# Optimization experiments

Hardware: AMD Instinct MI355X
Metric: run time of the kernel (lower is better)

The kernel has to match this reference:

```python
import jax, jax.numpy as jnp
import numpy as np

B, S, D = 4, 1024, 1024
DB = 128           # d_bottleneck (router embedding dim)
R = 128            # neuron bottleneck rank
N_QK, N_V, N_KNOW = 2048, 2048, 4096
MB_QK, MB_V, MB_KNOW = 16, 16, 32
H = 16
EPS = 1e-8


def _unit(k, shape):
    v = jax.random.normal(k, shape, jnp.float32)
    return v / (jnp.linalg.norm(v, axis=-1, keepdims=True) + EPS)


def setup_inputs() -> dict:
    key = jax.random.key(0)
    ks = jax.random.split(key, 16)
    s = 0.02
    nrm = lambda k, sh, sc=0.02: jax.random.normal(k, sh, jnp.float32) * sc
    return {
        "x": jax.random.normal(ks[0], (B, S, D), jnp.float32),
        "qk_emb": _unit(ks[1], (N_QK, DB)),
        "v_emb": _unit(ks[2], (N_V, DB)),
        "know_emb": _unit(ks[3], (N_KNOW, DB)),
        "qk_f": nrm(ks[4], (MB_QK, D, R)),
        "qk_r": nrm(ks[5], (MB_QK, R, D)),
        "v_f": nrm(ks[6], (MB_V, D, R)),
        "v_r": nrm(ks[7], (MB_V, R, D)),
        "know_f": nrm(ks[8], (MB_KNOW, D, R)),
        "know_r": nrm(ks[9], (MB_KNOW, R, D)),
        "proj_attn_k": nrm(ks[10], (D, 3 * DB)),
        "proj_attn_b": jnp.zeros((3 * DB,), jnp.float32),
        "tau_attn_k": nrm(ks[11], (D, 3)),
        "tau_attn_b": jnp.zeros((3,), jnp.float32),
        "proj_know_k": nrm(ks[12], (D, DB)),
        "proj_know_b": jnp.zeros((DB,), jnp.float32),
        "tau_know_k": nrm(ks[13], (D, 1)),
        "tau_know_b": jnp.zeros((1,), jnp.float32),
        "expand_O": nrm(ks[14], (D, D)),
        "ln1_scale": jnp.ones((D,), jnp.float32),
        "ln1_bias": jnp.zeros((D,), jnp.float32),
        "ln2_scale": jnp.ones((D,), jnp.float32),
        "ln2_bias": jnp.zeros((D,), jnp.float32),
    }


def layer_norm(x, scale, bias, eps=1e-6):
    mean = jnp.mean(x, axis=-1, keepdims=True)
    var = jnp.mean(jnp.square(x - mean), axis=-1, keepdims=True)
    return (x - mean) / jnp.sqrt(var + eps) * scale + bias


def threshold_gate(scores, tau):
    gate = jnp.maximum(scores - tau, 0.0)
    return gate / (gate.sum(axis=-1, keepdims=True) + EPS)


def group_gate(gate, n_basis):
    b, s, n = gate.shape  # n divisible by n_basis here
    g = gate.reshape(b, s, n_basis, n // n_basis).sum(axis=-1)
    return g / (g.sum(axis=-1, keepdims=True) + EPS)


@jax.checkpoint
def feature_fn(x, neurons, weights):
    all_h = jnp.einsum('bsd,ndr->bsnr', x, neurons)
    return jnp.einsum('bsnr,bsn->bsr', all_h, weights)


@jax.checkpoint
def restore_fn(h, neurons, weights):
    pre = jnp.einsum('bsr,bsn->bsnr', h, weights)
    return jnp.einsum('bsnr,nrd->bsd', pre, neurons)


def reference(x, qk_emb, v_emb, know_emb, qk_f, qk_r, v_f, v_r, know_f, know_r,
              proj_attn_k, proj_attn_b, tau_attn_k, tau_attn_b,
              proj_know_k, proj_know_b, tau_know_k, tau_know_b,
              expand_O, ln1_scale, ln1_bias, ln2_scale, ln2_bias):
    # ---- attention circuit (pre-LN) ----
    n1 = layer_norm(x, ln1_scale, ln1_bias)
    qk_n = qk_emb / (jnp.linalg.norm(qk_emb, axis=-1, keepdims=True) + EPS)
    v_n = v_emb / (jnp.linalg.norm(v_emb, axis=-1, keepdims=True) + EPS)
    h_all = n1 @ proj_attn_k + proj_attn_b            # [B,S,3*DB]
    h_q, h_k, h_v = jnp.split(h_all, 3, axis=-1)
    tau = n1 @ tau_attn_k + tau_attn_b                # [B,S,3]
    g_q = threshold_gate(h_q @ qk_n.T, tau[:, :, 0:1])
    g_k = threshold_gate(h_k @ qk_n.T, tau[:, :, 1:2])
    g_v = threshold_gate(h_v @ v_n.T, tau[:, :, 2:3])
    gq_b = group_gate(g_q, MB_QK)
    gk_b = group_gate(g_k, MB_QK)
    gv_b = group_gate(g_v, MB_V)
    Q = restore_fn(feature_fn(n1, qk_f, gq_b), qk_r, gq_b)
    K = restore_fn(feature_fn(n1, qk_f, gk_b), qk_r, gk_b)
    V = restore_fn(feature_fn(n1, v_f, gv_b), v_r, gv_b)
    d_head = D // H
    Q = Q.reshape(B, S, H, d_head).transpose(0, 2, 1, 3)
    K = K.reshape(B, S, H, d_head).transpose(0, 2, 1, 3)
    V = V.reshape(B, S, H, d_head).transpose(0, 2, 1, 3)
    scores = jnp.einsum('bhsd,bhtd->bhst', Q, K) / jnp.sqrt(jnp.float32(d_head))
    causal = jnp.tril(jnp.ones((S, S), dtype=jnp.bool_))
    scores = jnp.where(causal, scores, jnp.finfo(scores.dtype).min)
    attn_w = jax.nn.softmax(scores, axis=-1)
    attn_out = jnp.einsum('bhst,bhtd->bhsd', attn_w, V)
    attn_out = attn_out.transpose(0, 2, 1, 3).reshape(B, S, D) @ expand_O
    t_qk, t_v = 1.0 / N_QK, 1.0 / N_V
    a_aux = (((g_q.mean(axis=(0, 1)) - t_qk) ** 2).sum() * N_QK +
             ((g_k.mean(axis=(0, 1)) - t_qk) ** 2).sum() * N_QK +
             ((g_v.mean(axis=(0, 1)) - t_v) ** 2).sum() * N_V)
    x = x + attn_out
    # ---- knowledge circuit (pre-LN) ----
    n2 = layer_norm(x, ln2_scale, ln2_bias)
    know_n = know_emb / (jnp.linalg.norm(know_emb, axis=-1, keepdims=True) + EPS)
    h = n2 @ proj_know_k + proj_know_b
    tau_k = n2 @ tau_know_k + tau_know_b
    gate = threshold_gate(h @ know_n.T, tau_k)
    g_b = group_gate(gate, MB_KNOW)
    know_out = restore_fn(feature_fn(n2, know_f, g_b), know_r, g_b)
    k_aux = ((gate.mean(axis=(0, 1)) - 1.0 / N_KNOW) ** 2).sum() * N_KNOW
    x = x + know_out
    return x, a_aux + k_aux
```

## Files before the change

kernel.cpp:

```cpp
#include <hip/hip_runtime.h>
#include <math.h>

static constexpr int T = 4096;
static constexpr int D = 1024;

typedef __bf16 bf16_t;
typedef bf16_t bf16x8 __attribute__((ext_vector_type(8)));
typedef bf16_t bf16x4 __attribute__((ext_vector_type(4)));
typedef float f32x4 __attribute__((ext_vector_type(4)));

#define GLDS16(g, l)                                                        \
  __builtin_amdgcn_global_load_lds(                                         \
      (const __attribute__((address_space(1))) void*)(g),                   \
      (__attribute__((address_space(3))) void*)(l), 16, 0, 0)


__global__ void zero1_kernel(float* p) { *p = 0.f; }

__global__ __launch_bounds__(256) void ln_kernel(
    const float* __restrict__ x, const float* __restrict__ scale,
    const float* __restrict__ bias, float* __restrict__ out_f,
    bf16_t* __restrict__ out_b)
{
  int t = blockIdx.x;
  const float* xr = x + (size_t)t * D;
  float v[4];
  float s1 = 0.f, s2 = 0.f;
#pragma unroll
  for (int i = 0; i < 4; i++) {
    v[i] = xr[threadIdx.x + i * 256];
    s1 += v[i];
    s2 += v[i] * v[i];
  }
#pragma unroll
  for (int o = 1; o < 64; o <<= 1) {
    s1 += __shfl_xor(s1, o);
    s2 += __shfl_xor(s2, o);
  }
  __shared__ float r1[4], r2[4];
  int wid = threadIdx.x >> 6;
  if ((threadIdx.x & 63) == 0) { r1[wid] = s1; r2[wid] = s2; }
  __syncthreads();
  s1 = r1[0] + r1[1] + r1[2] + r1[3];
  s2 = r2[0] + r2[1] + r2[2] + r2[3];
  float mean = s1 * (1.f / D);
  float var = s2 * (1.f / D) - mean * mean;
  float rstd = rsqrtf(var + 1e-6f);
  float* orow = out_f + (size_t)t * D;
  bf16_t* brow = out_b + (size_t)t * D;
#pragma unroll
  for (int i = 0; i < 4; i++) {
    int d = threadIdx.x + i * 256;
    float o = (v[i] - mean) * rstd * scale[d] + bias[d];
    orow[d] = o;
    brow[d] = (bf16_t)o;
  }
}

__global__ __launch_bounds__(64) void norm_rows_kernel(
    const float* __restrict__ e, bf16_t* __restrict__ o)
{
  int r = blockIdx.x;
  const float* row = e + (size_t)r * 128;
  float a = row[threadIdx.x], b = row[threadIdx.x + 64];
  float ss = a * a + b * b;
#pragma unroll
  for (int m = 1; m < 64; m <<= 1) ss += __shfl_xor(ss, m);
  float inv = 1.f / (sqrtf(ss) + 1e-8f);
  bf16_t* orow = o + (size_t)r * 128;
  orow[threadIdx.x] = (bf16_t)(a * inv);
  orow[threadIdx.x + 64] = (bf16_t)(b * inv);
}

__global__ __launch_bounds__(64) void tau_kernel(
    const float* __restrict__ n, const float* __restrict__ W,
    const float* __restrict__ b, float* __restrict__ out, int J)
{
  int t = blockIdx.x;
  const float* nr = n + (size_t)t * D;
  for (int j = 0; j < J; j++) {
    float p = 0.f;
#pragma unroll 4
    for (int i = 0; i < 16; i++) {
      int d = threadIdx.x + i * 64;
      p += nr[d] * W[d * J + j];
    }
#pragma unroll
    for (int m = 1; m < 64; m <<= 1) p += __shfl_xor(p, m);
    if (threadIdx.x == 0) out[t * J + j] = p + b[j];
  }
}

template <int PER>
__device__ __forceinline__ void gate_body(
    float* __restrict__ row, float tv, float* __restrict__ gb, int G)
{
  float r[PER];
  int base = threadIdx.x * PER;
  float psum = 0.f;
#pragma unroll
  for (int i = 0; i < PER; i++) {
    float s = row[base + i] - tv;
    s = fmaxf(s, 0.f);
    r[i] = s;
    psum += s;
  }
  __shared__ float red[4];
  __shared__ float grp[32];
  if (threadIdx.x < 32) grp[threadIdx.x] = 0.f;
  float w = psum;
#pragma unroll
  for (int m = 1; m < 64; m <<= 1) w += __shfl_xor(w, m);
  int wid = threadIdx.x >> 6;
  if ((threadIdx.x & 63) == 0) red[wid] = w;
  __syncthreads();
  float Stot = red[0] + red[1] + red[2] + red[3];
  atomicAdd(&grp[base >> 7], psum);
  __syncthreads();
  float inv = 1.f / (Stot + 1e-8f);
#pragma unroll
  for (int i = 0; i < PER; i++) row[base + i] = r[i] * inv;
  if (threadIdx.x < G) {
    float Gj = grp[threadIdx.x] * inv;
    float gsum = Stot * inv;
    gb[threadIdx.x] = Gj / (gsum + 1e-8f);
  }
}

template <int PER>
__global__ __launch_bounds__(256) void gate_kernel(
    float* __restrict__ g, const float* __restrict__ tau, int tauStride,
    int tauOff, float* __restrict__ gb, int N, int G)
{
  int t = blockIdx.x;
  gate_body<PER>(g + (size_t)t * N, tau[t * tauStride + tauOff],
                 gb + (size_t)t * G, G);
}

template <int PER>
__global__ __launch_bounds__(256) void gate3_kernel(
    float* __restrict__ s0, float* __restrict__ s1, float* __restrict__ s2,
    const float* __restrict__ tau, float* __restrict__ g0,
    float* __restrict__ g1, float* __restrict__ g2, int N, int G)
{
  int t = blockIdx.x, y = blockIdx.y;
  float* g = y == 0 ? s0 : y == 1 ? s1 : s2;
  float* gb = y == 0 ? g0 : y == 1 ? g1 : g2;
  gate_body<PER>(g + (size_t)t * N, tau[t * 3 + y], gb + (size_t)t * G, G);
}

__global__ __launch_bounds__(256) void colsum_part_kernel(
    const float* __restrict__ g, int N, float* __restrict__ colsum)
{
  int c = blockIdx.x * 256 + threadIdx.x;
  int r0 = blockIdx.y * 128;
  const float* p = g + (size_t)r0 * N + c;
  float s = 0.f;
#pragma unroll 8
  for (int t = 0; t < 128; t++) s += p[(size_t)t * N];
  atomicAdd(&colsum[c], s);
}

__global__ __launch_bounds__(256) void colsum_part3_kernel(
    const float* __restrict__ s0, const float* __restrict__ s1,
    const float* __restrict__ s2, int N, float* __restrict__ colsum)
{
  int z = blockIdx.z;
  const float* g = z == 0 ? s0 : z == 1 ? s1 : s2;
  int c = blockIdx.x * 256 + threadIdx.x;
  int r0 = blockIdx.y * 128;
  const float* p = g + (size_t)r0 * N + c;
  float s = 0.f;
#pragma unroll 8
  for (int t = 0; t < 128; t++) s += p[(size_t)t * N];
  atomicAdd(&colsum[z * N + c], s);
}

__global__ __launch_bounds__(256) void colsum_fin_kernel(
    const float* __restrict__ colsum, int N, float tinv,
    float* __restrict__ aux)
{
  int c = blockIdx.x * 256 + threadIdx.x;
  float mdev = colsum[c] * (1.f / T) - tinv;
  float p = mdev * mdev * (float)N;
#pragma unroll
  for (int m = 1; m < 64; m <<= 1) p += __shfl_xor(p, m);
  __shared__ float red[4];
  if ((threadIdx.x & 63) == 0) red[threadIdx.x >> 6] = p;
  __syncthreads();
  if (threadIdx.x == 0) atomicAdd(aux, red[0] + red[1] + red[2] + red[3]);
}

__global__ __launch_bounds__(128) void wsum2_kernel(
    const bf16_t* __restrict__ all_h, const float* __restrict__ gb1,
    const float* __restrict__ gb2, float* __restrict__ h1,
    float* __restrict__ h2, int NB)
{
  int t = blockIdx.x;
  int r = threadIdx.x;
  const bf16_t* row = all_h + (size_t)t * NB * 128;
  float a1 = 0.f, a2 = 0.f;
  for (int n = 0; n < NB; n++) {
    float v = (float)row[n * 128 + r];
    a1 += gb1[(size_t)t * NB + n] * v;
    if (gb2) a2 += gb2[(size_t)t * NB + n] * v;
  }
  h1[(size_t)t * 128 + r] = a1;
  if (h2) h2[(size_t)t * 128 + r] = a2;
}

__global__ __launch_bounds__(128) void wsum2b_kernel(
    const bf16_t* __restrict__ aq, const bf16_t* __restrict__ av,
    const float* __restrict__ gq, const float* __restrict__ gk,
    const float* __restrict__ gv, float* __restrict__ hQ,
    float* __restrict__ hK, float* __restrict__ hV, int NB)
{
  int t = blockIdx.x, y = blockIdx.y;
  int r = threadIdx.x;
  const bf16_t* row = (y == 0 ? aq : av) + (size_t)t * NB * 128;
  const float* g1 = (y == 0 ? gq : gv) + (size_t)t * NB;
  const float* g2 = y == 0 ? gk + (size_t)t * NB : nullptr;
  float a1 = 0.f, a2 = 0.f;
  for (int n = 0; n < NB; n++) {
    float v = (float)row[n * 128 + r];
    a1 += g1[n] * v;
    if (g2) a2 += g2[n] * v;
  }
  if (y == 0) {
    hQ[(size_t)t * 128 + r] = a1;
    hK[(size_t)t * 128 + r] = a2;
  } else {
    hV[(size_t)t * 128 + r] = a1;
  }
}

__global__ __launch_bounds__(256) void transpose_to_bf16_kernel(
    const float* __restrict__ src, bf16_t* __restrict__ dst,
    int R, int C, size_t sbs, size_t dbs)
{
  __shared__ float tile[32][33];
  int b = blockIdx.z;
  int c0 = blockIdx.x * 32, r0 = blockIdx.y * 32;
  int tx = threadIdx.x & 31, ty = threadIdx.x >> 5;
  const float* s = src + (size_t)b * sbs;
  bf16_t* d = dst + (size_t)b * dbs;
#pragma unroll
  for (int i = 0; i < 4; i++)
    tile[ty + i * 8][tx] = s[(size_t)(r0 + ty + i * 8) * C + c0 + tx];
  __syncthreads();
#pragma unroll
  for (int i = 0; i < 4; i++)
    d[(size_t)(c0 + ty + i * 8) * R + r0 + tx] = (bf16_t)tile[tx][ty + i * 8];
}

__device__ __forceinline__ void avirt_body(
    const float* hr, const float* gr, bf16_t* ar, int K)
{
  int noct = K >> 3;
  for (int o = threadIdx.x; o < noct; o += 256) {
    int k = o * 8;
    float g = gr[k >> 7];
    bf16x8 v;
#pragma unroll
    for (int i = 0; i < 8; i++) v[i] = (bf16_t)(hr[(k & 127) + i] * g);
    *(bf16x8*)(ar + k) = v;
  }
}

__global__ __launch_bounds__(256) void avirt_kernel(
    const float* __restrict__ h, const float* __restrict__ gb, int NB,
    bf16_t* __restrict__ A, int K)
{
  int t = blockIdx.x;
  avirt_body(h + (size_t)t * 128, gb + (size_t)t * NB, A + (size_t)t * K, K);
}

__global__ __launch_bounds__(256) void avirt3_kernel(
    const float* __restrict__ h0, const float* __restrict__ h1,
    const float* __restrict__ h2, const float* __restrict__ g0,
    const float* __restrict__ g1, const float* __restrict__ g2, int NB,
    bf16_t* __restrict__ A0, bf16_t* __restrict__ A1,
    bf16_t* __restrict__ A2, int K)
{
  int t = blockIdx.x, y = blockIdx.y;
  const float* h = y == 0 ? h0 : y == 1 ? h1 : h2;
  const float* g = y == 0 ? g0 : y == 1 ? g1 : g2;
  bf16_t* A = y == 0 ? A0 : y == 1 ? A1 : A2;
  avirt_body(h + (size_t)t * 128, g + (size_t)t * NB, A + (size_t)t * K, K);
}

__global__ __launch_bounds__(256) void combine2_kernel(
    const float* __restrict__ p0, const float* __restrict__ p1,
    float* __restrict__ out)
{
  int i = blockIdx.x * 256 + threadIdx.x;
  float4 a = ((const float4*)p0)[i];
  float4 b = ((const float4*)p1)[i];
  float4 o = ((float4*)out)[i];
  o.x += a.x + b.x;
  o.y += a.y + b.y;
  o.z += a.z + b.z;
  o.w += a.w + b.w;
  ((float4*)out)[i] = o;
}

template <bool HAS_BIAS, bool HAS_RESID>
__device__ __forceinline__ void gemm_store(
    int mode, void* Cv, int ldc, const float* bias, const float* resid,
    int ldr, int rowb, int col, const f32x4& a)
{
  if (mode == 2) {
    bf16x4 v4;
#pragma unroll
    for (int r = 0; r < 4; r++) v4[r] = (bf16_t)a[r];
    bf16_t* dst = (bf16_t*)Cv +
        ((size_t)(rowb >> 10) * 1024 + col) * 1024 + (rowb & 1023);
    *(bf16x4*)dst = v4;
  } else {
#pragma unroll
    for (int r = 0; r < 4; r++) {
      int row = rowb + r;
      float v = a[r];
      if (HAS_BIAS) v += bias[col];
      if (HAS_RESID) v += resid[(size_t)row * ldr + col];
      if (mode == 1)
        ((bf16_t*)Cv)[(size_t)row * ldc + col] = (bf16_t)v;
      else
        ((float*)Cv)[(size_t)row * ldc + col] = v;
    }
  }
}

template <bool HAS_BIAS, bool HAS_RESID, int OUT_MODE>
__global__ __launch_bounds__(256) void mfma_gemm_kernel(
    const bf16_t* __restrict__ A, int lda,
    const bf16_t* __restrict__ Bt, int ldb,
    void* __restrict__ Cv, int ldc,
    const float* __restrict__ bias,
    const float* __restrict__ resid, int ldr,
    int M, int N, int K)
{
  __shared__ bf16_t As[2][64 * 32];
  __shared__ bf16_t Bs[2][128 * 32];
  int tid = threadIdx.x;
  int wave = tid >> 6, lane = tid & 63;

  unsigned lid = blockIdx.y * gridDim.x + blockIdx.x;
  unsigned nwg = gridDim.x * gridDim.y;
  unsigned swzb = lid;
  if ((nwg & 7u) == 0u) swzb = (lid & 7u) * (nwg >> 3) + (lid >> 3);
  int row0 = (int)(swzb / gridDim.x) * 64;
  int col0 = (int)(swzb % gridDim.x) * 128;

  int wr = (wave >> 1) * 32, wc = (wave & 1) * 64;
  f32x4 acc[2][4] = {};

  int srow = (wave << 4) + (lane >> 2);
  int g8 = (((lane & 3) ^ ((srow >> 1) & 3)) << 3);
  const bf16_t* gA = A + (size_t)(row0 + srow) * lda + g8;
  const bf16_t* gB = Bt + (size_t)(col0 + srow) * ldb + g8;
  size_t b64 = (size_t)64 * ldb;

  int fr = lane & 15, fq = lane >> 4;

#define GSTAGE(buf, k0s)                                  \
  {                                                       \
    GLDS16(gA + (k0s), &As[buf][wave * 512]);             \
    GLDS16(gB + (k0s), &Bs[buf][wave * 512]);             \
    GLDS16(gB + b64 + (k0s), &Bs[buf][2048 + wave * 512]);\
  }

  GSTAGE(0, 0);
  int cur = 0;
  for (int k0 = 0; k0 < K; k0 += 32) {
    __syncthreads();
    if (k0 + 32 < K) GSTAGE(cur ^ 1, k0 + 32);
    bf16x8 af[2], bfr[4];
#pragma unroll
    for (int m = 0; m < 2; m++) {
      int R = wr + m * 16 + fr;
      af[m] = *(const bf16x8*)&As[cur][R * 32 + ((fq ^ ((R >> 1) & 3)) << 3)];
    }
#pragma unroll
    for (int n = 0; n < 4; n++) {
      int R = wc + n * 16 + fr;
      bfr[n] = *(const bf16x8*)&Bs[cur][R * 32 + ((fq ^ ((R >> 1) & 3)) << 3)];
    }
#pragma unroll
    for (int m = 0; m < 2; m++)
#pragma unroll
      for (int n = 0; n < 4; n++)
        acc[m][n] = __builtin_amdgcn_mfma_f32_16x16x32_bf16(af[m], bfr[n],
                                                            acc[m][n], 0, 0, 0);
    cur ^= 1;
  }
#undef GSTAGE

#pragma unroll
  for (int m = 0; m < 2; m++)
#pragma unroll
    for (int n = 0; n < 4; n++)
      gemm_store<HAS_BIAS, HAS_RESID>(
          OUT_MODE, Cv, ldc, bias, resid, ldr,
          row0 + wr + m * 16 + fq * 4, col0 + wc + n * 16 + fr, acc[m][n]);
}

struct ZArg { const bf16_t* A; const bf16_t* Bt; void* C; int mode; };

__device__ __forceinline__ void gemm128_body(
    const bf16_t* __restrict__ A, int lda, const bf16_t* __restrict__ Bt,
    int ldb, void* __restrict__ Cv, int ldc, int mode, int row0, int col0,
    int K)
{
  __shared__ bf16_t As[2][128 * 32];
  __shared__ bf16_t Bs[2][128 * 32];
  int tid = threadIdx.x;
  int wave = tid >> 6, lane = tid & 63;
  int wr = (wave >> 1) * 64, wc = (wave & 1) * 64;
  f32x4 acc[4][4] = {};

  int srow = (wave << 4) + (lane >> 2);
  int g8 = (((lane & 3) ^ ((srow >> 1) & 3)) << 3);
  const bf16_t* gA = A + (size_t)(row0 + srow) * lda + g8;
  const bf16_t* gB = Bt + (size_t)(col0 + srow) * ldb + g8;
  size_t a64 = (size_t)64 * lda, b64 = (size_t)64 * ldb;

  int fr = lane & 15, fq = lane >> 4;

#define GSTAGE8(buf, k0s)                                  \
  {                                                        \
    GLDS16(gA + (k0s), &As[buf][wave * 512]);              \
    GLDS16(gA + a64 + (k0s), &As[buf][2048 + wave * 512]); \
    GLDS16(gB + (k0s), &Bs[buf][wave * 512]);              \
    GLDS16(gB + b64 + (k0s), &Bs[buf][2048 + wave * 512]); \
  }

  GSTAGE8(0, 0);
  int cur = 0;
  for (int k0 = 0; k0 < K; k0 += 32) {
    __syncthreads();
    if (k0 + 32 < K) GSTAGE8(cur ^ 1, k0 + 32);
    bf16x8 af[4], bfr[4];
#pragma unroll
    for (int m = 0; m < 4; m++) {
      int R = wr + m * 16 + fr;
      af[m] = *(const bf16x8*)&As[cur][R * 32 + ((fq ^ ((R >> 1) & 3)) << 3)];
    }
#pragma unroll
    for (int n = 0; n < 4; n++) {
      int R = wc + n * 16 + fr;
      bfr[n] = *(const bf16x8*)&Bs[cur][R * 32 + ((fq ^ ((R >> 1) & 3)) << 3)];
    }
#pragma unroll
    for (int m = 0; m < 4; m++)
#pragma unroll
      for (int n = 0; n < 4; n++)
        acc[m][n] = __builtin_amdgcn_mfma_f32_16x16x32_bf16(af[m], bfr[n],
                                                            acc[m][n], 0, 0, 0);
    cur ^= 1;
  }
#undef GSTAGE8

#pragma unroll
  for (int m = 0; m < 4; m++)
#pragma unroll
    for (int n = 0; n < 4; n++)
      gemm_store<false, false>(
          mode, Cv, ldc, nullptr, nullptr, 0,
          row0 + wr + m * 16 + fq * 4, col0 + wc + n * 16 + fr, acc[m][n]);
}

template <int OUT_MODE>
__global__ __launch_bounds__(256) void mfma_gemm128_kernel(
    const bf16_t* __restrict__ A, int lda,
    const bf16_t* __restrict__ Bt, int ldb,
    void* __restrict__ Cv, int ldc, int K)
{
  unsigned lid = blockIdx.y * gridDim.x + blockIdx.x;
  unsigned nwg = gridDim.x * gridDim.y;
  unsigned swzb = lid;
  if ((nwg & 7u) == 0u) swzb = (lid & 7u) * (nwg >> 3) + (lid >> 3);
  int row0 = (int)(swzb / gridDim.x) * 128;
  int col0 = (int)(swzb % gridDim.x) * 128;
  gemm128_body(A, lda, Bt, ldb, Cv, ldc, OUT_MODE, row0, col0, K);
}

__global__ __launch_bounds__(256) void mfma_gemm128b_kernel(
    ZArg za, ZArg zb, ZArg zc, int lda, int ldb, int ldc, int K)
{
  unsigned gx = gridDim.x;
  unsigned gxy = gridDim.x * gridDim.y;
  unsigned lid = (blockIdx.z * gridDim.y + blockIdx.y) * gx + blockIdx.x;
  unsigned nwg = gxy * gridDim.z;
  unsigned swzb = lid;
  if ((nwg & 7u) == 0u) swzb = (lid & 7u) * (nwg >> 3) + (lid >> 3);
  unsigned zi = swzb / gxy;
  unsigned rem = swzb % gxy;
  int row0 = (int)(rem / gx) * 128;
  int col0 = (int)(rem % gx) * 128;
  ZArg Z = (zi == 0) ? za : (zi == 1) ? zb : zc;
  gemm128_body(Z.A, lda, Z.Bt, ldb, Z.C, ldc, Z.mode, row0, col0, K);
}

__global__ __launch_bounds__(512) void flash_mfma_kernel(
    const bf16_t* __restrict__ Q, const bf16_t* __restrict__ K,
    const bf16_t* __restrict__ Vt, bf16_t* __restrict__ O)
{
  __shared__ bf16_t Ks[2][64 * 64];
  __shared__ bf16_t Vs[2][64 * 64];
  __shared__ bf16_t Pl[8][32 * 64];

  int tid = threadIdx.x;
  int wave = tid >> 6, lane = tid & 63;
  int fr = lane & 15, fq = lane >> 4;
  unsigned lid = blockIdx.x + blockIdx.y * 4 + blockIdx.z * 64;
  unsigned swz8 = (lid & 7u) * 32 + (lid >> 3);
  int s_slot = swz8 & 3;
  unsigned hb = swz8 >> 2;
  int h = hb & 15, b = hb >> 4;
  int half = wave >> 2, w4 = wave & 3;
  int qb = half ? (7 - s_slot) : s_slot;
  int q0w = qb * 128 + w4 * 32;
  int KT = 16 - 2 * s_slot;
  size_t qkbase = ((size_t)b * 1024) * 1024 + (size_t)h * 64;
  size_t vtbase = ((size_t)b * 1024 + (size_t)h * 64) * 1024;

  int srow8 = lane >> 3;
  int scb = (((lane & 7) << 4) ^ (srow8 << 4)) >> 1;

#define FSTAGE(buf, kt)                                                     \
  {                                                                         \
    int k0s = (kt) * 64;                                                    \
    int row = wave * 8 + srow8;                                             \
    GLDS16(&K[qkbase + (size_t)(k0s + row) * 1024 + scb],                   \
           &Ks[buf][wave * 512]);                                           \
    GLDS16(&Vt[vtbase + (size_t)row * 1024 + k0s + scb],                    \
           &Vs[buf][wave * 512]);                                           \
  }

  bf16x8 qf[2][2];
#pragma unroll
  for (int g = 0; g < 2; g++)
#pragma unroll
    for (int kh = 0; kh < 2; kh++)
      qf[g][kh] = *(const bf16x8*)&Q[qkbase +
                                     (size_t)(q0w + g * 16 + fr) * 1024 +
                                     kh * 32 + fq * 8];

  f32x4 o_acc[2][4] = {};
  float mrow[2][4], lrow[2][4];
#pragma unroll
  for (int g = 0; g < 2; g++)
#pragma unroll
    for (int r = 0; r < 4; r++) { mrow[g][r] = -INFINITY; lrow[g][r] = 0.f; }

  char* P = (char*)&Pl[wave][0];

  FSTAGE(0, 0);

  for (int kt = 0; kt < KT; kt++) {
    __syncthreads();
    if (kt + 1 < KT) FSTAGE((kt + 1) & 1, kt + 1);
    int k0 = kt * 64;
    if (k0 <= q0w + 31) {
      const char* Kb = (const char*)&Ks[kt & 1][0];
      const char* Vb = (const char*)&Vs[kt & 1][0];
      int swz = (fr & 7) << 4;
      f32x4 s[2][4] = {};
#pragma unroll
      for (int n = 0; n < 4; n++) {
        int rowo = (n * 16 + fr) * 128;
        bf16x8 kf0 = *(const bf16x8*)(Kb + rowo + ((fq * 16) ^ swz));
        bf16x8 kf1 = *(const bf16x8*)(Kb + rowo + ((64 + fq * 16) ^ swz));
#pragma unroll
        for (int g = 0; g < 2; g++) {
          s[g][n] = __builtin_amdgcn_mfma_f32_16x16x32_bf16(qf[g][0], kf0,
                                                            s[g][n], 0, 0, 0);
          s[g][n] = __builtin_amdgcn_mfma_f32_16x16x32_bf16(qf[g][1], kf1,
                                                            s[g][n], 0, 0, 0);
        }
      }
      const float scale = 0.125f;
#pragma unroll
      for (int g = 0; g < 2; g++) {
        bool dm = (k0 + 63 > q0w + g * 16);
#pragma unroll
        for (int n = 0; n < 4; n++)
#pragma unroll
          for (int r = 0; r < 4; r++) {
            float v = s[g][n][r] * scale;
            if (dm && (k0 + n * 16 + fr > q0w + g * 16 + fq * 4 + r))
              v = -INFINITY;
            s[g][n][r] = v;
          }
      }
      float corr[2][4];
#pragma unroll
      for (int g = 0; g < 2; g++)
#pragma unroll
        for (int r = 0; r < 4; r++) {
          float mx = fmaxf(fmaxf(s[g][0][r], s[g][1][r]),
                           fmaxf(s[g][2][r], s[g][3][r]));
#pragma unroll
          for (int msk = 1; msk < 16; msk <<= 1)
            mx = fmaxf(mx, __shfl_xor(mx, msk));
          float mnew = fmaxf(mrow[g][r], mx);
          corr[g][r] = __expf(mrow[g][r] - mnew);
          mrow[g][r] = mnew;
          float ps = 0.f;
#pragma unroll
          for (int n = 0; n < 4; n++) {
            float p = __expf(s[g][n][r] - mnew);
            s[g][n][r] = p;
            ps += p;
          }
#pragma unroll
          for (int msk = 1; msk < 16; msk <<= 1) ps += __shfl_xor(ps, msk);
          lrow[g][r] = lrow[g][r] * corr[g][r] + ps;
        }
#pragma unroll
      for (int g = 0; g < 2; g++)
#pragma unroll
        for (int n = 0; n < 4; n++)
#pragma unroll
          for (int r = 0; r < 4; r++) {
            int q = g * 16 + fq * 4 + r;
            int cb = ((n * 16 + fr) * 2) ^ ((q & 7) << 4);
            *(bf16_t*)(P + q * 128 + cb) = (bf16_t)s[g][n][r];
          }
      int rr = fr & 3;
      int srcl = (fr >> 2) << 4;
#pragma unroll
      for (int g = 0; g < 2; g++) {
        float c0 = __shfl(corr[g][0], srcl);
        float c1 = __shfl(corr[g][1], srcl);
        float c2 = __shfl(corr[g][2], srcl);
        float c3 = __shfl(corr[g][3], srcl);
        float cq = rr == 0 ? c0 : rr == 1 ? c1 : rr == 2 ? c2 : c3;
#pragma unroll
        for (int n = 0; n < 4; n++)
#pragma unroll
          for (int r = 0; r < 4; r++) o_acc[g][n][r] *= cq;
      }
#pragma unroll
      for (int c = 0; c < 2; c++) {
        bf16x8 pf[2];
#pragma unroll
        for (int g = 0; g < 2; g++)
          pf[g] = *(const bf16x8*)(P + (g * 16 + fr) * 128 +
                                   ((c * 64 + fq * 16) ^ swz));
#pragma unroll
        for (int n = 0; n < 4; n++) {
          bf16x8 vf = *(const bf16x8*)(Vb + (n * 16 + fr) * 128 +
                                       ((c * 64 + fq * 16) ^ swz));
#pragma unroll
          for (int g = 0; g < 2; g++)
            o_acc[g][n] = __builtin_amdgcn_mfma_f32_16x16x32_bf16(
                vf, pf[g], o_acc[g][n], 0, 0, 0);
        }
      }
    }
  }
  int rr = fr & 3;
  int srcl = (fr >> 2) << 4;
#pragma unroll
  for (int g = 0; g < 2; g++) {
    float l0 = __shfl(lrow[g][0], srcl);
    float l1 = __shfl(lrow[g][1], srcl);
    float l2 = __shfl(lrow[g][2], srcl);
    float l3 = __shfl(lrow[g][3], srcl);
    float lq = rr == 0 ? l0 : rr == 1 ? l1 : rr == 2 ? l2 : l3;
    float linv = 1.f / lq;
    size_t orow = qkbase + (size_t)(q0w + g * 16 + fr) * 1024;
#pragma unroll
    for (int n = 0; n < 4; n++) {
      bf16x4 ov;
#pragma unroll
      for (int r = 0; r < 4; r++) ov[r] = (bf16_t)(o_acc[g][n][r] * linv);
      *(bf16x4*)&O[orow + n * 16 + fq * 4] = ov;
    }
  }
#undef FSTAGE
}


extern "C" void kernel_launch(void* const* d_in, const int* in_sizes, int n_in,
                              void* d_out, int out_size, void* d_ws,
                              size_t ws_size, hipStream_t stream) {
  (void)in_sizes; (void)n_in; (void)out_size; (void)ws_size;
  const float* x          = (const float*)d_in[0];
  const float* qk_emb     = (const float*)d_in[1];
  const float* v_emb      = (const float*)d_in[2];
  const float* know_emb   = (const float*)d_in[3];
  const float* qk_f       = (const float*)d_in[4];
  const float* qk_r       = (const float*)d_in[5];
  const float* v_f        = (const float*)d_in[6];
  const float* v_r        = (const float*)d_in[7];
  const float* know_f     = (const float*)d_in[8];
  const float* know_r     = (const float*)d_in[9];
  const float* proj_attn_k = (const float*)d_in[10];
  const float* proj_attn_b = (const float*)d_in[11];
  const float* tau_attn_k  = (const float*)d_in[12];
  const float* tau_attn_b  = (const float*)d_in[13];
  const float* proj_know_k = (const float*)d_in[14];
  const float* proj_know_b = (const float*)d_in[15];
  const float* tau_know_k  = (const float*)d_in[16];
  const float* tau_know_b  = (const float*)d_in[17];
  const float* expand_O    = (const float*)d_in[18];
  const float* ln1_scale   = (const float*)d_in[19];
  const float* ln1_bias    = (const float*)d_in[20];
  const float* ln2_scale   = (const float*)d_in[21];
  const float* ln2_bias    = (const float*)d_in[22];

  float* out = (float*)d_out;
  float* aux = out + (size_t)T * D;

  float* ws = (float*)d_ws;
  float* n_f   = ws;
  float* tau3  = n_f + 4194304;
  float* gq_b  = tau3 + 16384;
  float* gk_b  = gq_b + 65536;
  float* gv_b  = gk_b + 65536;
  float* gkn_b = gv_b + 65536;
  float* csum  = gkn_b + 131072;
  float* hQ    = csum + 8192;
  float* hK    = hQ + 524288;
  float* hV    = hK + 524288;
  float* qkvarena = hV + 524288;
  float* buf_big = qkvarena + 12582912;

  bf16_t* Qbb = (bf16_t*)qkvarena;
  bf16_t* Kbb = Qbb + (size_t)T * 1024;
  bf16_t* Vtb = Kbb + (size_t)T * 1024;

  bf16_t* nb   = (bf16_t*)(buf_big + 16777216);
  bf16_t* hab  = nb + 4194304;
  bf16_t* embB = hab + 1572864;
  bf16_t* B2t  = embB + 524288;
  bf16_t* wt   = B2t + 4194304;
  bf16_t* pa_t  = wt;
  bf16_t* qkr_t = pa_t + 393216;
  bf16_t* vr_t  = qkr_t + 2097152;
  bf16_t* knr_t = vr_t + 2097152;
  bf16_t* eo_t  = knr_t + 4194304;
  bf16_t* pk_t  = eo_t + 1048576;
  bf16_t* B2t2  = pk_t + 131072;

  float* s_q = buf_big;
  float* s_k = buf_big + 8388608;
  float* s_v = (float*)qkvarena;
  bf16_t* allh_q = (bf16_t*)buf_big;
  bf16_t* allh_v = allh_q + (size_t)T * 2048;
  bf16_t* avbQ = (bf16_t*)buf_big;
  bf16_t* avbK = avbQ + (size_t)T * 2048;
  bf16_t* avbV = avbK + (size_t)T * 2048;
  bf16_t* avbN = (bf16_t*)buf_big;
  bf16_t* allh_n = (bf16_t*)buf_big;
  float* kp0 = buf_big + 8388608;
  float* kp1 = kp0 + 4194304;
  bf16_t* attnb_b = (bf16_t*)(buf_big + 12582912);

  bf16_t* embQ = embB;
  bf16_t* embV = embB + 262144;

  dim3 blk(256);

  zero1_kernel<<<1, 1, 0, stream>>>(aux);

  transpose_to_bf16_kernel<<<dim3(12, 32, 1), blk, 0, stream>>>(
      proj_attn_k, pa_t, 1024, 384, 0, 0);
  transpose_to_bf16_kernel<<<dim3(32, 64, 1), blk, 0, stream>>>(
      qk_r, qkr_t, 2048, 1024, 0, 0);
  transpose_to_bf16_kernel<<<dim3(32, 64, 1), blk, 0, stream>>>(
      v_r, vr_t, 2048, 1024, 0, 0);
  transpose_to_bf16_kernel<<<dim3(32, 128, 1), blk, 0, stream>>>(
      know_r, knr_t, 4096, 1024, 0, 0);
  transpose_to_bf16_kernel<<<dim3(32, 32, 1), blk, 0, stream>>>(
      expand_O, eo_t, 1024, 1024, 0, 0);
  transpose_to_bf16_kernel<<<dim3(4, 32, 1), blk, 0, stream>>>(
      proj_know_k, pk_t, 1024, 128, 0, 0);
  transpose_to_bf16_kernel<<<dim3(4, 32, 16), blk, 0, stream>>>(
      qk_f, B2t, 1024, 128, 131072, 131072);
  transpose_to_bf16_kernel<<<dim3(4, 32, 16), blk, 0, stream>>>(
      v_f, B2t2, 1024, 128, 131072, 131072);

  ln_kernel<<<T, blk, 0, stream>>>(x, ln1_scale, ln1_bias, n_f, nb);
  norm_rows_kernel<<<2048, 64, 0, stream>>>(qk_emb, embQ);
  norm_rows_kernel<<<2048, 64, 0, stream>>>(v_emb, embV);

  mfma_gemm_kernel<true, false, 1><<<dim3(3, 64), blk, 0, stream>>>(
      nb, 1024, pa_t, 1024, hab, 384, proj_attn_b, nullptr, 0, T, 384, 1024);
  tau_kernel<<<T, 64, 0, stream>>>(n_f, tau_attn_k, tau_attn_b, tau3, 3);

  {
    ZArg zq{hab + 0, embQ, s_q, 0};
    ZArg zk{hab + 128, embQ, s_k, 0};
    ZArg zv{hab + 256, embV, s_v, 0};
    mfma_gemm128b_kernel<<<dim3(16, 32, 3), blk, 0, stream>>>(
        zq, zk, zv, 384, 128, 2048, 128);
  }
  gate3_kernel<8><<<dim3(T, 3), blk, 0, stream>>>(
      s_q, s_k, s_v, tau3, gq_b, gk_b, gv_b, 2048, 16);
  hipMemsetAsync(csum, 0, 6144 * sizeof(float), stream);
  colsum_part3_kernel<<<dim3(8, 32, 3), blk, 0, stream>>>(s_q, s_k, s_v,
                                                          2048, csum);
  colsum_fin_kernel<<<24, blk, 0, stream>>>(csum, 2048, 1.f / 2048.f, aux);

  {
    ZArg zf1{nb, B2t, allh_q, 1};
    ZArg zf2{nb, B2t2, allh_v, 1};
    mfma_gemm128b_kernel<<<dim3(16, 32, 2), blk, 0, stream>>>(
        zf1, zf2, zf1, 1024, 1024, 2048, 1024);
  }
  wsum2b_kernel<<<dim3(T, 2), 128, 0, stream>>>(allh_q, allh_v, gq_b, gk_b,
                                                gv_b, hQ, hK, hV, 16);

  avirt3_kernel<<<dim3(T, 3), blk, 0, stream>>>(hQ, hK, hV, gq_b, gk_b, gv_b,
                                                16, avbQ, avbK, avbV, 2048);
  {
    ZArg zq{avbQ, qkr_t, Qbb, 1};
    ZArg zk{avbK, qkr_t, Kbb, 1};
    ZArg zv{avbV, vr_t, Vtb, 2};
    mfma_gemm128b_kernel<<<dim3(8, 32, 3), blk, 0, stream>>>(
        zq, zk, zv, 2048, 2048, 1024, 2048);
  }

  flash_mfma_kernel<<<dim3(4, 16, 4), dim3(512), 0, stream>>>(Qbb, Kbb, Vtb,
                                                              attnb_b);
  mfma_gemm_kernel<false, true, 0><<<dim3(8, 64), blk, 0, stream>>>(
      attnb_b, 1024, eo_t, 1024, out, 1024, nullptr, x, 1024, T, 1024, 1024);

  ln_kernel<<<T, blk, 0, stream>>>(out, ln2_scale, ln2_bias, n_f, nb);
  norm_rows_kernel<<<4096, 64, 0, stream>>>(know_emb, embB);
  mfma_gemm_kernel<true, false, 1><<<dim3(1, 64), blk, 0, stream>>>(
      nb, 1024, pk_t, 1024, hab, 128, proj_know_b, nullptr, 0, T, 128, 1024);
  tau_kernel<<<T, 64, 0, stream>>>(n_f, tau_know_k, tau_know_b, tau3, 1);

  mfma_gemm128_kernel<0><<<dim3(32, 32), blk, 0, stream>>>(
      hab, 128, embB, 128, buf_big, 4096, 128);
  gate_kernel<16><<<T, blk, 0, stream>>>(buf_big, tau3, 1, 0, gkn_b, 4096, 32);
  hipMemsetAsync(csum, 0, 4096 * sizeof(float), stream);
  colsum_part_kernel<<<dim3(16, 32), blk, 0, stream>>>(buf_big, 4096, csum);
  colsum_fin_kernel<<<16, blk, 0, stream>>>(csum, 4096, 1.f / 4096.f, aux);

  transpose_to_bf16_kernel<<<dim3(4, 32, 32), blk, 0, stream>>>(
      know_f, B2t, 1024, 128, 131072, 131072);
  mfma_gemm128_kernel<1><<<dim3(32, 32), blk, 0, stream>>>(
      nb, 1024, B2t, 1024, allh_n, 4096, 1024);
  wsum2_kernel<<<T, 128, 0, stream>>>(allh_n, gkn_b, nullptr, hQ, nullptr, 32);

  avirt_kernel<<<T, blk, 0, stream>>>(hQ, gkn_b, 32, avbN, 4096);
  {
    ZArg z0{avbN, knr_t, kp0, 0};
    ZArg z1{avbN + 2048, knr_t + 2048, kp1, 0};
    mfma_gemm128b_kernel<<<dim3(8, 32, 2), blk, 0, stream>>>(
        z0, z1, z0, 4096, 4096, 1024, 2048);
  }
  combine2_kernel<<<4096, blk, 0, stream>>>(kp0, kp1, out);
}
```

Before: 589.3 us.

## Store router scores as bf16 and recompute gates in colsum instead of writing back

The router score GEMMs now emit bf16 instead of fp32, halving the score matrix traffic. The gate kernels no longer write normalized gates back to memory. They only store a per-row inverse sum, and the column-sum kernels recompute relu(score - tau) * inv on the fly. This removes a full read-write pass over large score matrices, but the scores lose precision from the bf16 rounding, which could shift threshold decisions and the aux loss slightly.

Result: faster. 563.8 us (-4.3%).

```diff
diff --git a/kernel.cpp b/kernel.cpp
--- a/kernel.cpp
+++ b/kernel.cpp
@@ -92,18 +92,17 @@
 }
 
 template <int PER>
-__device__ __forceinline__ void gate_body(
-    float* __restrict__ row, float tv, float* __restrict__ gb, int G)
-{
-  float r[PER];
+__device__ __forceinline__ void gateb_body(
+    const bf16_t* __restrict__ row, float tv, float* __restrict__ gb, int G,
+    float* __restrict__ rowinv)
+{
   int base = threadIdx.x * PER;
   float psum = 0.f;
 #pragma unroll
-  for (int i = 0; i < PER; i++) {
-    float s = row[base + i] - tv;
-    s = fmaxf(s, 0.f);
-    r[i] = s;
-    psum += s;
+  for (int i = 0; i < PER; i += 8) {
+    bf16x8 v = *(const bf16x8*)(row + base + i);
+#pragma unroll
+    for (int j = 0; j < 8; j++) psum += fmaxf((float)v[j] - tv, 0.f);
   }
   __shared__ float red[4];
   __shared__ float grp[32];
@@ -118,8 +117,7 @@
   atomicAdd(&grp[base >> 7], psum);
   __syncthreads();
   float inv = 1.f / (Stot + 1e-8f);
-#pragma unroll
-  for (int i = 0; i < PER; i++) row[base + i] = r[i] * inv;
+  if (threadIdx.x == 0) *rowinv = inv;
   if (threadIdx.x < G) {
     float Gj = grp[threadIdx.x] * inv;
     float gsum = Stot * inv;
@@ -128,52 +126,62 @@
 }
 
 template <int PER>
-__global__ __launch_bounds__(256) void gate_kernel(
-    float* __restrict__ g, const float* __restrict__ tau, int tauStride,
-    int tauOff, float* __restrict__ gb, int N, int G)
+__global__ __launch_bounds__(256) void gate3b_kernel(
+    const bf16_t* __restrict__ s0, const bf16_t* __restrict__ s1,
+    const bf16_t* __restrict__ s2, const float* __restrict__ tau,
+    float* __restrict__ g0, float* __restrict__ g1, float* __restrict__ g2,
+    float* __restrict__ ri, int N, int G)
+{
+  int t = blockIdx.x, y = blockIdx.y;
+  const bf16_t* g = y == 0 ? s0 : y == 1 ? s1 : s2;
+  float* gb = y == 0 ? g0 : y == 1 ? g1 : g2;
+  gateb_body<PER>(g + (size_t)t * N, tau[t * 3 + y], gb + (size_t)t * G, G,
+                  ri + (size_t)y * T + t);
+}
+
+template <int PER>
+__global__ __launch_bounds__(256) void gateb_kernel(
+    const bf16_t* __restrict__ s, const float* __restrict__ tau,
+    float* __restrict__ gb, float* __restrict__ ri, int N, int G)
 {
   int t = blockIdx.x;
-  gate_body<PER>(g + (size_t)t * N, tau[t * tauStride + tauOff],
-                 gb + (size_t)t * G, G);
-}
-
-template <int PER>
-__global__ __launch_bounds__(256) void gate3_kernel(
-    float* __restrict__ s0, float* __restrict__ s1, float* __restrict__ s2,
-    const float* __restrict__ tau, float* __restrict__ g0,
-    float* __restrict__ g1, float* __restrict__ g2, int N, int G)
-{
-  int t = blockIdx.x, y = blockIdx.y;
-  float* g = y == 0 ? s0 : y == 1 ? s1 : s2;
-  float* gb = y == 0 ? g0 : y == 1 ? g1 : g2;
-  gate_body<PER>(g + (size_t)t * N, tau[t * 3 + y], gb + (size_t)t * G, G);
-}
-
-__global__ __launch_bounds__(256) void colsum_part_kernel(
-    const float* __restrict__ g, int N, float* __restrict__ colsum)
-{
+  gateb_body<PER>(s + (size_t)t * N, tau[t], gb + (size_t)t * G, G, ri + t);
+}
+
+__global__ __launch_bounds__(256) void colsumb_part3_kernel(
+    const bf16_t* __restrict__ s0, const bf16_t* __restrict__ s1,
+    const bf16_t* __restrict__ s2, const float* __restrict__ tau,
+    const float* __restrict__ ri, int N, float* __restrict__ colsum)
+{
+  int z = blockIdx.z;
+  const bf16_t* g = z == 0 ? s0 : z == 1 ? s1 : s2;
+  const float* riz = ri + (size_t)z * T;
   int c = blockIdx.x * 256 + threadIdx.x;
   int r0 = blockIdx.y * 128;
-  const float* p = g + (size_t)r0 * N + c;
   float s = 0.f;
-#pragma unroll 8
-  for (int t = 0; t < 128; t++) s += p[(size_t)t * N];
-  atomicAdd(&colsum[c], s);
-}
-
-__global__ __launch_bounds__(256) void colsum_part3_kernel(
-    const float* __restrict__ s0, const float* __restrict__ s1,
-    const float* __restrict__ s2, int N, float* __restrict__ colsum)
-{
-  int z = blockIdx.z;
-  const float* g = z == 0 ? s0 : z == 1 ? s1 : s2;
+#pragma unroll 4
+  for (int t = 0; t < 128; t++) {
+    int row = r0 + t;
+    float v = (float)g[(size_t)row * N + c];
+    s += fmaxf(v - tau[row * 3 + z], 0.f) * riz[row];
+  }
+  atomicAdd(&colsum[z * N + c], s);
+}
+
+__global__ __launch_bounds__(256) void colsumb_part_kernel(
+    const bf16_t* __restrict__ g, const float* __restrict__ tau,
+    const float* __restrict__ ri, int N, float* __restrict__ colsum)
+{
   int c = blockIdx.x * 256 + threadIdx.x;
   int r0 = blockIdx.y * 128;
-  const float* p = g + (size_t)r0 * N + c;
   float s = 0.f;
-#pragma unroll 8
-  for (int t = 0; t < 128; t++) s += p[(size_t)t * N];
-  atomicAdd(&colsum[z * N + c], s);
+#pragma unroll 4
+  for (int t = 0; t < 128; t++) {
+    int row = r0 + t;
+    float v = (float)g[(size_t)row * N + c];
+    s += fmaxf(v - tau[row], 0.f) * ri[row];
+  }
+  atomicAdd(&colsum[c], s);
 }
 
 __global__ __launch_bounds__(256) void colsum_fin_kernel(
@@ -723,7 +731,8 @@
   float* gv_b  = gk_b + 65536;
   float* gkn_b = gv_b + 65536;
   float* csum  = gkn_b + 131072;
-  float* hQ    = csum + 8192;
+  float* rinv  = csum + 8192;
+  float* hQ    = rinv + 16384;
   float* hK    = hQ + 524288;
   float* hV    = hK + 524288;
   float* qkvarena = hV + 524288;
@@ -746,9 +755,10 @@
   bf16_t* pk_t  = eo_t + 1048576;
   bf16_t* B2t2  = pk_t + 131072;
 
-  float* s_q = buf_big;
-  float* s_k = buf_big + 8388608;
-  float* s_v = (float*)qkvarena;
+  bf16_t* s_qb = (bf16_t*)buf_big;
+  bf16_t* s_kb = s_qb + (size_t)T * 2048;
+  bf16_t* s_vb = s_kb + (size_t)T * 2048;
+  bf16_t* kscb = (bf16_t*)buf_big;
   bf16_t* allh_q = (bf16_t*)buf_big;
   bf16_t* allh_v = allh_q + (size_t)T * 2048;
   bf16_t* avbQ = (bf16_t*)buf_big;
@@ -793,17 +803,17 @@
   tau_kernel<<<T, 64, 0, stream>>>(n_f, tau_attn_k, tau_attn_b, tau3, 3);
 
   {
-    ZArg zq{hab + 0, embQ, s_q, 0};
-    ZArg zk{hab + 128, embQ, s_k, 0};
-    ZArg zv{hab + 256, embV, s_v, 0};
+    ZArg zq{hab + 0, embQ, s_qb, 1};
+    ZArg zk{hab + 128, embQ, s_kb, 1};
+    ZArg zv{hab + 256, embV, s_vb, 1};
     mfma_gemm128b_kernel<<<dim3(16, 32, 3), blk, 0, stream>>>(
         zq, zk, zv, 384, 128, 2048, 128);
   }
-  gate3_kernel<8><<<dim3(T, 3), blk, 0, stream>>>(
-      s_q, s_k, s_v, tau3, gq_b, gk_b, gv_b, 2048, 16);
+  gate3b_kernel<8><<<dim3(T, 3), blk, 0, stream>>>(
+      s_qb, s_kb, s_vb, tau3, gq_b, gk_b, gv_b, rinv, 2048, 16);
   hipMemsetAsync(csum, 0, 6144 * sizeof(float), stream);
-  colsum_part3_kernel<<<dim3(8, 32, 3), blk, 0, stream>>>(s_q, s_k, s_v,
-                                                          2048, csum);
+  colsumb_part3_kernel<<<dim3(8, 32, 3), blk, 0, stream>>>(
+      s_qb, s_kb, s_vb, tau3, rinv, 2048, csum);
   colsum_fin_kernel<<<24, blk, 0, stream>>>(csum, 2048, 1.f / 2048.f, aux);
 
   {
@@ -836,11 +846,13 @@
       nb, 1024, pk_t, 1024, hab, 128, proj_know_b, nullptr, 0, T, 128, 1024);
   tau_kernel<<<T, 64, 0, stream>>>(n_f, tau_know_k, tau_know_b, tau3, 1);
 
-  mfma_gemm128_kernel<0><<<dim3(32, 32), blk, 0, stream>>>(
-      hab, 128, embB, 128, buf_big, 4096, 128);
-  gate_kernel<16><<<T, blk, 0, stream>>>(buf_big, tau3, 1, 0, gkn_b, 4096, 32);
+  mfma_gemm128_kernel<1><<<dim3(32, 32), blk, 0, stream>>>(
+      hab, 128, embB, 128, kscb, 4096, 128);
+  gateb_kernel<16><<<T, blk, 0, stream>>>(kscb, tau3, gkn_b, rinv + 3 * T,
+                                          4096, 32);
   hipMemsetAsync(csum, 0, 4096 * sizeof(float), stream);
-  colsum_part_kernel<<<dim3(16, 32), blk, 0, stream>>>(buf_big, 4096, csum);
+  colsumb_part_kernel<<<dim3(16, 32), blk, 0, stream>>>(
+      kscb, tau3, rinv + 3 * T, 4096, csum);
   colsum_fin_kernel<<<16, blk, 0, stream>>>(csum, 4096, 1.f / 4096.f, aux);
 
   transpose_to_bf16_kernel<<<dim3(4, 32, 32), blk, 0, stream>>>(
```
